# Kernel tuning notes

Hardware: AMD Instinct MI355X
Metric: run time of the kernel (lower is better)

## Reference

```python
import jax, jax.numpy as jnp
import numpy as np

B, S, DIM, N_CONCEPTS, N_LAYERS = 4, 2048, 1024, 2048, 2


def _phase_linear(x, W, b):
    # x: [b,s,d_in,2]; same real linear applied to real and imag components
    return jnp.einsum('bsdp,od->bsop', x, W) + b[:, None]


def _phase_layernorm(x, gamma, beta, eps=1e-5):
    # per-component LayerNorm over the feature dim with shared affine params
    mu = x.mean(axis=-2, keepdims=True)
    var = x.var(axis=-2, keepdims=True)
    return (x - mu) / jnp.sqrt(var + eps) * gamma[:, None] + beta[:, None]


def setup_inputs() -> dict:
    key = jax.random.key(0)
    ks = jax.random.split(key, 8)
    x = jax.random.normal(ks[0], (B, S, DIM, 2), dtype=jnp.float32)
    concept_memory = jax.random.normal(ks[1], (N_CONCEPTS, DIM, 2), dtype=jnp.float32) * 0.02
    scale = 1.0 / np.sqrt(DIM)
    W_layers = jax.random.normal(ks[2], (N_LAYERS, DIM, DIM), dtype=jnp.float32) * scale
    b_layers = jnp.zeros((N_LAYERS, DIM), dtype=jnp.float32)
    gamma = jnp.ones((N_LAYERS, DIM), dtype=jnp.float32)
    beta = jnp.zeros((N_LAYERS, DIM), dtype=jnp.float32)
    W_out = jax.random.normal(ks[3], (DIM, DIM), dtype=jnp.float32) * scale
    b_out = jnp.zeros((DIM,), dtype=jnp.float32)
    g_out = jnp.ones((DIM,), dtype=jnp.float32)
    beta_out = jnp.zeros((DIM,), dtype=jnp.float32)
    return {"x": x, "concept_memory": concept_memory, "W_layers": W_layers,
            "b_layers": b_layers, "gamma": gamma, "beta": beta,
            "W_out": W_out, "b_out": b_out, "g_out": g_out, "beta_out": beta_out}


def reference(x, concept_memory, W_layers, b_layers, gamma, beta, W_out, b_out, g_out, beta_out):
    xr, xi = x[..., 0], x[..., 1]                       # [b,s,d]
    cr, ci = concept_memory[..., 0], concept_memory[..., 1]  # [n,d]
    # phase-coherence concept attention
    dot_real = jnp.einsum('bsd,nd->bsn', xr, cr) + jnp.einsum('bsd,nd->bsn', xi, ci)
    x_mag = jnp.sqrt((xr ** 2 + xi ** 2).sum(axis=-1, keepdims=True) + 1e-8)   # [b,s,1]
    c_mag = jnp.sqrt((cr ** 2 + ci ** 2).sum(axis=-1) + 1e-8)                  # [n]
    coherence = dot_real / (x_mag * c_mag[None, None, :] + 1e-8)
    concept_attn = jax.nn.softmax(coherence * 2.0, axis=-1)
    concept_retrieved = jnp.einsum('bsn,ndp->bsdp', concept_attn, concept_memory)
    h = x + concept_retrieved * 0.1
    # gated FFN blocks (eval mode: dropout off)
    for l in range(N_LAYERS):
        residual = h
        h = _phase_layernorm(h, gamma[l], beta[l])
        h = _phase_linear(h, W_layers[l], b_layers[l])
        h = jax.nn.gelu(h[..., 0:1], approximate=False) * h
        h = residual + h * 0.1
    out = _phase_layernorm(h, g_out, beta_out)
    out = _phase_linear(out, W_out, b_out)
    return out
```

## Files before the change

kernel.cpp:

```cpp
#include <hip/hip_runtime.h>
#include <hip/hip_bf16.h>

#define ROWS 8192
#define K2   2048
#define NCPT 2048
#define DIMD 1024

using short8 = __attribute__((ext_vector_type(8))) short;
using f32x4  = __attribute__((ext_vector_type(4))) float;

__device__ __forceinline__ unsigned short f2b(float f) {
  __hip_bfloat16 h = __float2bfloat16(f);
  return *reinterpret_cast<unsigned short*>(&h);
}
__device__ __forceinline__ float b2f(unsigned short u) {
  unsigned int x = ((unsigned int)u) << 16;
  return __uint_as_float(x);
}

__device__ __forceinline__ void store_bf16x8(unsigned short* dst, const float4& a, const float4& b) {
  union { unsigned short u[8]; uint4 q; } p;
  p.u[0]=f2b(a.x); p.u[1]=f2b(a.y); p.u[2]=f2b(a.z); p.u[3]=f2b(a.w);
  p.u[4]=f2b(b.x); p.u[5]=f2b(b.y); p.u[6]=f2b(b.z); p.u[7]=f2b(b.w);
  *reinterpret_cast<uint4*>(dst) = p.q;
}
__device__ __forceinline__ void store_bf16x4(unsigned short* dst, float a, float b, float c, float d) {
  union { unsigned short u[4]; uint2 q; } p;
  p.u[0]=f2b(a); p.u[1]=f2b(b); p.u[2]=f2b(c); p.u[3]=f2b(d);
  *reinterpret_cast<uint2*>(dst) = p.q;
}

__device__ __forceinline__ void async_lds16(const void* g, void* l) {
  __builtin_amdgcn_global_load_lds((__attribute__((address_space(1))) void*)g,
                                   (__attribute__((address_space(3))) void*)l, 16, 0, 0);
}

__global__ void cast_row_mag(const float* __restrict__ src, unsigned short* __restrict__ dst,
                             float* __restrict__ mag, int ncol) {
  __shared__ float sred[4];
  int row = blockIdx.x, t = threadIdx.x;
  const float* s = src + (size_t)row * ncol;
  unsigned short* d = dst + (size_t)row * ncol;
  float ss = 0.f;
  for (int i = t * 8; i < ncol; i += 2048) {
    float4 a = *(const float4*)(s + i);
    float4 b = *(const float4*)(s + i + 4);
    ss += a.x*a.x + a.y*a.y + a.z*a.z + a.w*a.w;
    ss += b.x*b.x + b.y*b.y + b.z*b.z + b.w*b.w;
    store_bf16x8(d + i, a, b);
  }
  int lane = t & 63, w = t >> 6;
  for (int o = 32; o; o >>= 1) ss += __shfl_down(ss, o);
  if (lane == 0) sred[w] = ss;
  __syncthreads();
  if (t == 0) mag[row] = sqrtf(sred[0] + sred[1] + sred[2] + sred[3] + 1e-8f);
}

__global__ void cast_w(const float* __restrict__ wl, const float* __restrict__ wo,
                       unsigned short* __restrict__ dst) {
  int b = blockIdx.x;
  const float* src;
  unsigned short* d;
  if (b < 1024) { src = wl + (size_t)b * 2048; d = dst + (size_t)b * 2048; }
  else {
    src = wo + (size_t)(b - 1024) * 2048;
    d = dst + (size_t)2 * 1024 * 1024 + (size_t)(b - 1024) * 2048;
  }
  int i = threadIdx.x * 8;
  float4 a = *(const float4*)(src + i);
  float4 c = *(const float4*)(src + i + 4);
  store_bf16x8(d + i, a, c);
}

__global__ void transpose_f2b(const float* __restrict__ src, unsigned short* __restrict__ dst, int n) {
  __shared__ float tile[32][33];
  int bx = blockIdx.x * 32;
  int by = blockIdx.y * 32;
  int tx = threadIdx.x & 31, ty = threadIdx.x >> 5;
  #pragma unroll
  for (int i = ty; i < 32; i += 8)
    tile[i][tx] = src[(size_t)(by + i) * n + bx + tx];
  __syncthreads();
  #pragma unroll
  for (int i = ty; i < 32; i += 8)
    dst[(size_t)(bx + i) * n + by + tx] = f2b(tile[tx][i]);
}

__global__ void softmax_attn(const unsigned short* __restrict__ logit, unsigned short* __restrict__ attn) {
  __shared__ float sred[4];
  int row = blockIdx.x, t = threadIdx.x;
  int lane = t & 63, w = t >> 6;
  const unsigned short* lr = logit + (size_t)row * NCPT + t * 8;
  short8 lv = *reinterpret_cast<const short8*>(lr);
  float l[8];
  #pragma unroll
  for (int i = 0; i < 8; ++i) l[i] = b2f((unsigned short)lv[i]);
  float m = l[0];
  #pragma unroll
  for (int i = 1; i < 8; ++i) m = fmaxf(m, l[i]);
  for (int o = 32; o; o >>= 1) m = fmaxf(m, __shfl_down(m, o));
  if (lane == 0) sred[w] = m;
  __syncthreads();
  m = fmaxf(fmaxf(sred[0], sred[1]), fmaxf(sred[2], sred[3]));
  __syncthreads();
  float e[8], s = 0.f;
  #pragma unroll
  for (int i = 0; i < 8; ++i) { e[i] = expf(l[i] - m); s += e[i]; }
  for (int o = 32; o; o >>= 1) s += __shfl_down(s, o);
  if (lane == 0) sred[w] = s;
  __syncthreads();
  s = sred[0] + sred[1] + sred[2] + sred[3];
  float inv = 1.f / s;
  float4 A = make_float4(e[0]*inv, e[1]*inv, e[2]*inv, e[3]*inv);
  float4 B = make_float4(e[4]*inv, e[5]*inv, e[6]*inv, e[7]*inv);
  store_bf16x8(attn + (size_t)row * NCPT + t * 8, A, B);
}

__global__ void phase_ln(const unsigned short* __restrict__ h, const float* __restrict__ gamma,
                         const float* __restrict__ beta, unsigned short* __restrict__ out) {
  __shared__ float4 s4[4];
  int bs = blockIdx.x, t = threadIdx.x;
  const unsigned short* hr = h + (size_t)bs * 2048 + t * 8;
  short8 hv = *reinterpret_cast<const short8*>(hr);
  float r0 = b2f((unsigned short)hv[0]), i0 = b2f((unsigned short)hv[1]);
  float r1 = b2f((unsigned short)hv[2]), i1 = b2f((unsigned short)hv[3]);
  float r2 = b2f((unsigned short)hv[4]), i2 = b2f((unsigned short)hv[5]);
  float r3 = b2f((unsigned short)hv[6]), i3 = b2f((unsigned short)hv[7]);
  float4 s;
  s.x = r0 + r1 + r2 + r3;
  s.y = r0*r0 + r1*r1 + r2*r2 + r3*r3;
  s.z = i0 + i1 + i2 + i3;
  s.w = i0*i0 + i1*i1 + i2*i2 + i3*i3;
  int lane = t & 63, w = t >> 6;
  for (int o = 32; o; o >>= 1) {
    s.x += __shfl_down(s.x, o); s.y += __shfl_down(s.y, o);
    s.z += __shfl_down(s.z, o); s.w += __shfl_down(s.w, o);
  }
  if (lane == 0) s4[w] = s;
  __syncthreads();
  float4 T = s4[0];
  #pragma unroll
  for (int i = 1; i < 4; ++i) { T.x += s4[i].x; T.y += s4[i].y; T.z += s4[i].z; T.w += s4[i].w; }
  const float invd = 1.f / 1024.f;
  float mu_r = T.x * invd, var_r = T.y * invd - mu_r * mu_r;
  float mu_i = T.z * invd, var_i = T.w * invd - mu_i * mu_i;
  float is_r = 1.f / sqrtf(var_r + 1e-5f);
  float is_i = 1.f / sqrtf(var_i + 1e-5f);
  float4 g = *(const float4*)(gamma + t * 4);
  float4 b = *(const float4*)(beta + t * 4);
  unsigned short* o0 = out + (size_t)(2 * bs) * 1024 + t * 4;
  unsigned short* o1 = out + (size_t)(2 * bs + 1) * 1024 + t * 4;
  store_bf16x4(o0, (r0-mu_r)*is_r*g.x + b.x, (r1-mu_r)*is_r*g.y + b.y,
                   (r2-mu_r)*is_r*g.z + b.z, (r3-mu_r)*is_r*g.w + b.w);
  store_bf16x4(o1, (i0-mu_i)*is_i*g.x + b.x, (i1-mu_i)*is_i*g.y + b.y,
                   (i2-mu_i)*is_i*g.z + b.z, (i3-mu_i)*is_i*g.w + b.w);
}

template <int EPI>
__global__ __launch_bounds__(512, 2) void gemm256(
    const unsigned short* __restrict__ A, const unsigned short* __restrict__ B,
    int M, int N, int K, void* __restrict__ Cv, const float* __restrict__ aux,
    const float* __restrict__ aux2, const unsigned short* __restrict__ auxb) {
  __shared__ char lds[131072];
  const int t = threadIdx.x;
  const int l = t & 63;
  const int wid = t >> 6;
  const int wm = wid >> 2, wn = wid & 3;

  const int nwg = gridDim.x * gridDim.y;
  int bid = blockIdx.y * gridDim.x + blockIdx.x;
  const int chunk = nwg >> 3;
  bid = (bid & 7) * chunk + (bid >> 3);
  const int row0 = (bid / gridDim.x) * 256;
  const int col0 = (bid % gridDim.x) * 256;

  const int NT = K >> 6;
  const int l15 = l & 15, l7 = l & 7, lk = l >> 4;

  f32x4 acc[8][4] = {};
  short8 afA[4][2];
  short8 bfA[2][2];
  short8 bfB[2][2];

  auto stage = [&](const unsigned short* gmat, int tileRow, int kcol, char* region) {
    const int rsub = t >> 3;
    const int csw = ((t & 7) ^ (rsub & 7)) << 3;
    const unsigned short* g0 = gmat + (size_t)(tileRow + rsub) * K + kcol + csw;
    async_lds16(g0, region + (t & ~63) * 16);
    async_lds16(g0 + (size_t)64 * K, region + 8192 + (t & ~63) * 16);
  };

  auto rdA = [&](const char* base, int m, int kh) -> short8 {
    const int r = wm * 64 + m * 16 + l15;
    const int sp = ((((kh << 2) | lk) ^ l7) << 4);
    return *reinterpret_cast<const short8*>(base + r * 128 + sp);
  };
  auto rdB = [&](const char* base, int n, int kh) -> short8 {
    const int r = wn * 32 + n * 16 + l15;
    const int sp = ((((kh << 2) | lk) ^ l7) << 4);
    return *reinterpret_cast<const short8*>(base + r * 128 + sp);
  };

  stage(A, row0,       0, lds + 0);
  stage(A, row0 + 128, 0, lds + 16384);
  stage(B, col0,       0, lds + 32768);
  stage(B, col0 + 128, 0, lds + 49152);
  if (NT > 1) {
    stage(A, row0,       64, lds + 65536 + 0);
    stage(A, row0 + 128, 64, lds + 65536 + 16384);
    stage(B, col0,       64, lds + 65536 + 32768);
    stage(B, col0 + 128, 64, lds + 65536 + 49152);
    asm volatile("s_waitcnt vmcnt(8)" ::: "memory");
  } else {
    asm volatile("s_waitcnt vmcnt(0)" ::: "memory");
  }
  __builtin_amdgcn_s_barrier();
  asm volatile("" ::: "memory");

  #pragma unroll
  for (int n = 0; n < 2; ++n)
    #pragma unroll
    for (int kh = 0; kh < 2; ++kh)
      bfA[n][kh] = rdB(lds + 32768, n, kh);

  for (int tk = 0; tk < NT; ++tk) {
    char* bufC = lds + (tk & 1) * 65536;
    char* bufN = lds + (((tk + 1) & 1) * 65536);
    const bool pf = (tk + 2 < NT);
    const int kpf = (tk + 2) * 64;

    #pragma unroll
    for (int m = 0; m < 4; ++m)
      #pragma unroll
      for (int kh = 0; kh < 2; ++kh)
        afA[m][kh] = rdA(bufC + 0, m, kh);
    __builtin_amdgcn_s_setprio(1);
    #pragma unroll
    for (int kh = 0; kh < 2; ++kh)
      #pragma unroll
      for (int m = 0; m < 4; ++m)
        #pragma unroll
        for (int n = 0; n < 2; ++n)
          acc[m][n] = __builtin_amdgcn_mfma_f32_16x16x32_bf16(afA[m][kh], bfA[n][kh], acc[m][n], 0, 0, 0);
    __builtin_amdgcn_s_setprio(0);
    #pragma unroll
    for (int n = 0; n < 2; ++n)
      #pragma unroll
      for (int kh = 0; kh < 2; ++kh)
        bfB[n][kh] = rdB(bufC + 49152, n, kh);
    asm volatile("" ::: "memory");
    __builtin_amdgcn_s_barrier();
    asm volatile("" ::: "memory");

    __builtin_amdgcn_s_setprio(1);
    #pragma unroll
    for (int kh = 0; kh < 2; ++kh)
      #pragma unroll
      for (int m = 0; m < 4; ++m)
        #pragma unroll
        for (int n = 0; n < 2; ++n)
          acc[m][n + 2] = __builtin_amdgcn_mfma_f32_16x16x32_bf16(afA[m][kh], bfB[n][kh], acc[m][n + 2], 0, 0, 0);
    __builtin_amdgcn_s_setprio(0);
    if (pf) {
      stage(A, row0, kpf, bufC + 0);
      stage(B, col0, kpf, bufC + 32768);
    }
    asm volatile("" ::: "memory");
    __builtin_amdgcn_s_barrier();
    asm volatile("" ::: "memory");

    #pragma unroll
    for (int m = 0; m < 4; ++m)
      #pragma unroll
      for (int kh = 0; kh < 2; ++kh)
        afA[m][kh] = rdA(bufC + 16384, m, kh);
    __builtin_amdgcn_s_setprio(1);
    #pragma unroll
    for (int kh = 0; kh < 2; ++kh)
      #pragma unroll
      for (int m = 0; m < 4; ++m)
        #pragma unroll
        for (int n = 0; n < 2; ++n)
          acc[m + 4][n] = __builtin_amdgcn_mfma_f32_16x16x32_bf16(afA[m][kh], bfA[n][kh], acc[m + 4][n], 0, 0, 0);
    __builtin_amdgcn_s_setprio(0);
    if (pf) stage(B, col0 + 128, kpf, bufC + 49152);
    asm volatile("" ::: "memory");
    __builtin_amdgcn_s_barrier();
    asm volatile("" ::: "memory");

    __builtin_amdgcn_s_setprio(1);
    #pragma unroll
    for (int kh = 0; kh < 2; ++kh)
      #pragma unroll
      for (int m = 0; m < 4; ++m)
        #pragma unroll
        for (int n = 0; n < 2; ++n)
          acc[m + 4][n + 2] = __builtin_amdgcn_mfma_f32_16x16x32_bf16(afA[m][kh], bfB[n][kh], acc[m + 4][n + 2], 0, 0, 0);
    __builtin_amdgcn_s_setprio(0);
    if (pf) stage(A, row0 + 128, kpf, bufC + 16384);
    if (tk + 1 < NT) {
      #pragma unroll
      for (int n = 0; n < 2; ++n)
        #pragma unroll
        for (int kh = 0; kh < 2; ++kh)
          bfA[n][kh] = rdB(bufN + 32768, n, kh);
    }
    if (pf) {
      asm volatile("s_waitcnt vmcnt(4)" ::: "memory");
    } else {
      asm volatile("s_waitcnt vmcnt(0)" ::: "memory");
    }
    __builtin_amdgcn_s_barrier();
    asm volatile("" ::: "memory");
  }
  asm volatile("s_waitcnt vmcnt(0)" ::: "memory");

  const int cr = lk * 4;
  #pragma unroll
  for (int m = 0; m < 8; ++m) {
    const int gr = row0 + ((m >> 2) << 7) + wm * 64 + ((m & 3) << 4) + cr;
    #pragma unroll
    for (int n = 0; n < 4; ++n) {
      const int gc = col0 + ((n >> 1) << 7) + wn * 32 + ((n & 1) << 4) + l15;
      if constexpr (EPI == 0) {
        unsigned short* C = (unsigned short*)Cv;
        const float cm_ = aux2[gc];
        #pragma unroll
        for (int j = 0; j < 4; ++j) {
          const int r = gr + j;
          float v = 2.f * acc[m][n][j] / (aux[r] * cm_ + 1e-8f);
          C[(size_t)r * N + gc] = f2b(v);
        }
      } else if constexpr (EPI == 1) {
        unsigned short* C = (unsigned short*)Cv;
        #pragma unroll
        for (int j = 0; j < 4; ++j) {
          const int r = gr + j;
          C[(size_t)r * N + gc] = f2b(b2f(auxb[(size_t)r * N + gc]) + 0.1f * acc[m][n][j]);
        }
      } else if constexpr (EPI == 2) {
        unsigned short* C = (unsigned short*)Cv;
        const float bb = aux[gc];
        #pragma unroll
        for (int jj = 0; jj < 2; ++jj) {
          const int r = gr + jj * 2;
          float re = acc[m][n][jj * 2] + bb;
          float im = acc[m][n][jj * 2 + 1] + bb;
          float g = 0.5f * re * (1.f + erff(re * 0.70710678118654752440f));
          size_t idx = (size_t)(r >> 1) * 2048 + (size_t)gc * 2;
          unsigned int hv = *(unsigned int*)(C + idx);
          float hx = b2f((unsigned short)(hv & 0xffff));
          float hy = b2f((unsigned short)(hv >> 16));
          hx += 0.1f * g * re;
          hy += 0.1f * g * im;
          unsigned int packed = (unsigned int)f2b(hx) | ((unsigned int)f2b(hy) << 16);
          *(unsigned int*)(C + idx) = packed;
        }
      } else {
        float* C = (float*)Cv;
        const float bb = aux[gc];
        const size_t idx0 = (size_t)(gr >> 1) * 2048 + (size_t)gc * 2;
        float2 v01 = make_float2(acc[m][n][0] + bb, acc[m][n][1] + bb);
        float2 v23 = make_float2(acc[m][n][2] + bb, acc[m][n][3] + bb);
        *(float2*)(C + idx0) = v01;
        *(float2*)(C + idx0 + 2048) = v23;
      }
    }
  }
}

extern "C" void kernel_launch(void* const* d_in, const int* in_sizes, int n_in,
                              void* d_out, int out_size, void* d_ws, size_t ws_size,
                              hipStream_t stream) {
  const float* x     = (const float*)d_in[0];
  const float* cm    = (const float*)d_in[1];
  const float* Wl    = (const float*)d_in[2];
  const float* bl    = (const float*)d_in[3];
  const float* gamma = (const float*)d_in[4];
  const float* beta  = (const float*)d_in[5];
  const float* Wo    = (const float*)d_in[6];
  const float* bo    = (const float*)d_in[7];
  const float* go    = (const float*)d_in[8];
  const float* bto   = (const float*)d_in[9];
  float* out = (float*)d_out;

  char* p = (char*)d_ws;
  unsigned short* x_bf = (unsigned short*)p; p += (size_t)ROWS * K2 * 2;
  unsigned short* c_bf = (unsigned short*)p; p += (size_t)NCPT * K2 * 2;
  unsigned short* c_T  = (unsigned short*)p; p += (size_t)K2 * NCPT * 2;
  unsigned short* w_bf = (unsigned short*)p; p += (size_t)3 * 1024 * 1024 * 2;
  float* x_mag = (float*)p; p += (size_t)ROWS * 4;
  float* c_mag = (float*)p; p += (size_t)NCPT * 4;
  unsigned short* dot_bf = (unsigned short*)p; p += (size_t)ROWS * NCPT * 2;
  unsigned short* attn   = (unsigned short*)p; p += (size_t)ROWS * NCPT * 2;
  unsigned short* h      = (unsigned short*)p; p += (size_t)ROWS * K2 * 2;
  unsigned short* ln_bf = attn;

  cast_row_mag<<<ROWS, 256, 0, stream>>>(x, x_bf, x_mag, K2);
  cast_row_mag<<<NCPT, 256, 0, stream>>>(cm, c_bf, c_mag, K2);
  transpose_f2b<<<dim3(64, 64), 256, 0, stream>>>(cm, c_T, 2048);
  cast_w<<<1536, 256, 0, stream>>>(Wl, Wo, w_bf);

  gemm256<0><<<dim3(NCPT / 256, ROWS / 256), 512, 0, stream>>>(
      x_bf, c_bf, ROWS, NCPT, K2, dot_bf, x_mag, c_mag, nullptr);
  softmax_attn<<<ROWS, 256, 0, stream>>>(dot_bf, attn);
  gemm256<1><<<dim3(K2 / 256, ROWS / 256), 512, 0, stream>>>(
      attn, c_T, ROWS, K2, NCPT, h, nullptr, nullptr, x_bf);

  for (int l = 0; l < 2; ++l) {
    phase_ln<<<ROWS, 256, 0, stream>>>(h, gamma + l * 1024, beta + l * 1024, ln_bf);
    gemm256<2><<<dim3(DIMD / 256, 2 * ROWS / 256), 512, 0, stream>>>(
        ln_bf, w_bf + (size_t)l * 1024 * 1024, 2 * ROWS, DIMD, DIMD, h, bl + l * 1024, nullptr, nullptr);
  }

  phase_ln<<<ROWS, 256, 0, stream>>>(h, go, bto, ln_bf);
  gemm256<3><<<dim3(DIMD / 256, 2 * ROWS / 256), 512, 0, stream>>>(
      ln_bf, w_bf + 2 * 1024 * 1024, 2 * ROWS, DIMD, DIMD, out, bo, nullptr, nullptr);
}
```

Measured before the change: 362.5 us.

## Restructure GEMM main loop into eight-phase ping-pong with explicit LDS waits

Reworks the 256x256 bf16 MFMA GEMM main loop so each of the four quadrant MFMA blocks is preceded by its own LDS reads and global prefetch stage, separated by barriers with explicit lgkmcnt waits and sched_barrier fences. The B-fragment preload across iterations is removed; B fragments are now read from the current buffer at the start of each iteration. The aim is a tighter ping-pong schedule where memory issue and MFMA bursts alternate between wave groups. It adds more barriers per iteration and changes the vmcnt wait count, which could add synchronization stalls.

```diff
diff --git a/kernel.cpp b/kernel.cpp
--- a/kernel.cpp
+++ b/kernel.cpp
@@ -178,9 +178,9 @@
   const int l15 = l & 15, l7 = l & 7, lk = l >> 4;
 
   f32x4 acc[8][4] = {};
-  short8 afA[4][2];
-  short8 bfA[2][2];
-  short8 bfB[2][2];
+  short8 a_[4][2];
+  short8 b0_[2][2];
+  short8 b1_[2][2];
 
   auto stage = [&](const unsigned short* gmat, int tileRow, int kcol, char* region) {
     const int rsub = t >> 3;
@@ -217,15 +217,8 @@
   __builtin_amdgcn_s_barrier();
   asm volatile("" ::: "memory");
 
-  #pragma unroll
-  for (int n = 0; n < 2; ++n)
-    #pragma unroll
-    for (int kh = 0; kh < 2; ++kh)
-      bfA[n][kh] = rdB(lds + 32768, n, kh);
-
   for (int tk = 0; tk < NT; ++tk) {
     char* bufC = lds + (tk & 1) * 65536;
-    char* bufN = lds + (((tk + 1) & 1) * 65536);
     const bool pf = (tk + 2 < NT);
     const int kpf = (tk + 2) * 64;
 
@@ -233,7 +226,16 @@
     for (int m = 0; m < 4; ++m)
       #pragma unroll
       for (int kh = 0; kh < 2; ++kh)
-        afA[m][kh] = rdA(bufC + 0, m, kh);
+        a_[m][kh] = rdA(bufC + 0, m, kh);
+    #pragma unroll
+    for (int n = 0; n < 2; ++n)
+      #pragma unroll
+      for (int kh = 0; kh < 2; ++kh)
+        b0_[n][kh] = rdB(bufC + 32768, n, kh);
+    asm volatile("s_waitcnt lgkmcnt(8)" ::: "memory");
+    __builtin_amdgcn_s_barrier();
+    asm volatile("s_waitcnt lgkmcnt(0)" ::: "memory");
+    __builtin_amdgcn_sched_barrier(0);
     __builtin_amdgcn_s_setprio(1);
     #pragma unroll
     for (int kh = 0; kh < 2; ++kh)
@@ -241,30 +243,33 @@
       for (int m = 0; m < 4; ++m)
         #pragma unroll
         for (int n = 0; n < 2; ++n)
-          acc[m][n] = __builtin_amdgcn_mfma_f32_16x16x32_bf16(afA[m][kh], bfA[n][kh], acc[m][n], 0, 0, 0);
+          acc[m][n] = __builtin_amdgcn_mfma_f32_16x16x32_bf16(a_[m][kh], b0_[n][kh], acc[m][n], 0, 0, 0);
     __builtin_amdgcn_s_setprio(0);
+    asm volatile("" ::: "memory");
+    __builtin_amdgcn_s_barrier();
+    asm volatile("" ::: "memory");
+
     #pragma unroll
     for (int n = 0; n < 2; ++n)
       #pragma unroll
       for (int kh = 0; kh < 2; ++kh)
-        bfB[n][kh] = rdB(bufC + 49152, n, kh);
-    asm volatile("" ::: "memory");
-    __builtin_amdgcn_s_barrier();
-    asm volatile("" ::: "memory");
-
-    __builtin_amdgcn_s_setprio(1);
-    #pragma unroll
-    for (int kh = 0; kh < 2; ++kh)
-      #pragma unroll
-      for (int m = 0; m < 4; ++m)
-        #pragma unroll
-        for (int n = 0; n < 2; ++n)
-          acc[m][n + 2] = __builtin_amdgcn_mfma_f32_16x16x32_bf16(afA[m][kh], bfB[n][kh], acc[m][n + 2], 0, 0, 0);
-    __builtin_amdgcn_s_setprio(0);
+        b1_[n][kh] = rdB(bufC + 49152, n, kh);
     if (pf) {
       stage(A, row0, kpf, bufC + 0);
       stage(B, col0, kpf, bufC + 32768);
     }
+    __builtin_amdgcn_s_barrier();
+    asm volatile("s_waitcnt lgkmcnt(0)" ::: "memory");
+    __builtin_amdgcn_sched_barrier(0);
+    __builtin_amdgcn_s_setprio(1);
+    #pragma unroll
+    for (int kh = 0; kh < 2; ++kh)
+      #pragma unroll
+      for (int m = 0; m < 4; ++m)
+        #pragma unroll
+        for (int n = 0; n < 2; ++n)
+          acc[m][n + 2] = __builtin_amdgcn_mfma_f32_16x16x32_bf16(a_[m][kh], b1_[n][kh], acc[m][n + 2], 0, 0, 0);
+    __builtin_amdgcn_s_setprio(0);
     asm volatile("" ::: "memory");
     __builtin_amdgcn_s_barrier();
     asm volatile("" ::: "memory");
@@ -273,7 +278,11 @@
     for (int m = 0; m < 4; ++m)
       #pragma unroll
       for (int kh = 0; kh < 2; ++kh)
-        afA[m][kh] = rdA(bufC + 16384, m, kh);
+        a_[m][kh] = rdA(bufC + 16384, m, kh);
+    if (pf) stage(B, col0 + 128, kpf, bufC + 49152);
+    __builtin_amdgcn_s_barrier();
+    asm volatile("s_waitcnt lgkmcnt(0)" ::: "memory");
+    __builtin_amdgcn_sched_barrier(0);
     __builtin_amdgcn_s_setprio(1);
     #pragma unroll
     for (int kh = 0; kh < 2; ++kh)
@@ -281,35 +290,30 @@
       for (int m = 0; m < 4; ++m)
         #pragma unroll
         for (int n = 0; n < 2; ++n)
-          acc[m + 4][n] = __builtin_amdgcn_mfma_f32_16x16x32_bf16(afA[m][kh], bfA[n][kh], acc[m + 4][n], 0, 0, 0);
+          acc[m + 4][n] = __builtin_amdgcn_mfma_f32_16x16x32_bf16(a_[m][kh], b0_[n][kh], acc[m + 4][n], 0, 0, 0);
     __builtin_amdgcn_s_setprio(0);
-    if (pf) stage(B, col0 + 128, kpf, bufC + 49152);
-    asm volatile("" ::: "memory");
-    __builtin_amdgcn_s_barrier();
-    asm volatile("" ::: "memory");
-
-    __builtin_amdgcn_s_setprio(1);
-    #pragma unroll
-    for (int kh = 0; kh < 2; ++kh)
-      #pragma unroll
-      for (int m = 0; m < 4; ++m)
-        #pragma unroll
-        for (int n = 0; n < 2; ++n)
-          acc[m + 4][n + 2] = __builtin_amdgcn_mfma_f32_16x16x32_bf16(afA[m][kh], bfB[n][kh], acc[m + 4][n + 2], 0, 0, 0);
-    __builtin_amdgcn_s_setprio(0);
-    if (pf) stage(A, row0 + 128, kpf, bufC + 16384);
-    if (tk + 1 < NT) {
-      #pragma unroll
-      for (int n = 0; n < 2; ++n)
-        #pragma unroll
-        for (int kh = 0; kh < 2; ++kh)
-          bfA[n][kh] = rdB(bufN + 32768, n, kh);
-    }
+    asm volatile("" ::: "memory");
+    __builtin_amdgcn_s_barrier();
+    asm volatile("" ::: "memory");
+
     if (pf) {
-      asm volatile("s_waitcnt vmcnt(4)" ::: "memory");
+      stage(A, row0 + 128, kpf, bufC + 16384);
+      asm volatile("s_waitcnt vmcnt(6)" ::: "memory");
     } else {
       asm volatile("s_waitcnt vmcnt(0)" ::: "memory");
     }
+    __builtin_amdgcn_s_barrier();
+    asm volatile("" ::: "memory");
+    __builtin_amdgcn_s_setprio(1);
+    #pragma unroll
+    for (int kh = 0; kh < 2; ++kh)
+      #pragma unroll
+      for (int m = 0; m < 4; ++m)
+        #pragma unroll
+        for (int n = 0; n < 2; ++n)
+          acc[m + 4][n + 2] = __builtin_amdgcn_mfma_f32_16x16x32_bf16(a_[m][kh], b1_[n][kh], acc[m + 4][n + 2], 0, 0, 0);
+    __builtin_amdgcn_s_setprio(0);
+    asm volatile("" ::: "memory");
     __builtin_amdgcn_s_barrier();
     asm volatile("" ::: "memory");
   }
```

Measured after the change: 390.4 us. +7.7%, slower.

## Run concept attention GEMMs in FP8 with scaled MFMA

Applied to the files above, without the earlier changes.

Converts x, the concept memory, its transpose and the softmax attention weights to FP8 e4m3, with power-of-two prescales (16 for concepts, 256 for attention) undone in the epilogues. Adds a new gemm256f8 kernel that uses the 16x16x128 f8f6f4 scaled MFMA with 128-wide K tiles, replacing the two bf16 GEMMs of the attention stage. This halves operand bytes and raises matrix throughput, at the cost of reduced precision in the coherence logits and in the retrieved concepts.

```diff
diff --git a/kernel.cpp b/kernel.cpp
--- a/kernel.cpp
+++ b/kernel.cpp
@@ -1,5 +1,6 @@
 #include <hip/hip_runtime.h>
 #include <hip/hip_bf16.h>
+#include <hip/hip_fp8.h>
 
 #define ROWS 8192
 #define K2   2048
@@ -8,6 +9,7 @@
 
 using short8 = __attribute__((ext_vector_type(8))) short;
 using f32x4  = __attribute__((ext_vector_type(4))) float;
+using int8v  = __attribute__((ext_vector_type(8))) int;
 
 __device__ __forceinline__ unsigned short f2b(float f) {
   __hip_bfloat16 h = __float2bfloat16(f);
@@ -16,6 +18,10 @@
 __device__ __forceinline__ float b2f(unsigned short u) {
   unsigned int x = ((unsigned int)u) << 16;
   return __uint_as_float(x);
+}
+__device__ __forceinline__ unsigned char f2f8(float f) {
+  __hip_fp8_e4m3 h(f);
+  return (unsigned char)h.__x;
 }
 
 __device__ __forceinline__ void store_bf16x8(unsigned short* dst, const float4& a, const float4& b) {
@@ -29,25 +35,32 @@
   p.u[0]=f2b(a); p.u[1]=f2b(b); p.u[2]=f2b(c); p.u[3]=f2b(d);
   *reinterpret_cast<uint2*>(dst) = p.q;
 }
+__device__ __forceinline__ void store_fp8x8(unsigned char* dst, const float4& a, const float4& b, float s) {
+  union { unsigned char c[8]; uint2 q; } p;
+  p.c[0]=f2f8(a.x*s); p.c[1]=f2f8(a.y*s); p.c[2]=f2f8(a.z*s); p.c[3]=f2f8(a.w*s);
+  p.c[4]=f2f8(b.x*s); p.c[5]=f2f8(b.y*s); p.c[6]=f2f8(b.z*s); p.c[7]=f2f8(b.w*s);
+  *reinterpret_cast<uint2*>(dst) = p.q;
+}
 
 __device__ __forceinline__ void async_lds16(const void* g, void* l) {
   __builtin_amdgcn_global_load_lds((__attribute__((address_space(1))) void*)g,
                                    (__attribute__((address_space(3))) void*)l, 16, 0, 0);
 }
 
-__global__ void cast_row_mag(const float* __restrict__ src, unsigned short* __restrict__ dst,
+__global__ void cast_row_mag(const float* __restrict__ src, unsigned short* __restrict__ dst_bf,
+                             unsigned char* __restrict__ dst_f8, float fscale,
                              float* __restrict__ mag, int ncol) {
   __shared__ float sred[4];
   int row = blockIdx.x, t = threadIdx.x;
   const float* s = src + (size_t)row * ncol;
-  unsigned short* d = dst + (size_t)row * ncol;
   float ss = 0.f;
   for (int i = t * 8; i < ncol; i += 2048) {
     float4 a = *(const float4*)(s + i);
     float4 b = *(const float4*)(s + i + 4);
     ss += a.x*a.x + a.y*a.y + a.z*a.z + a.w*a.w;
     ss += b.x*b.x + b.y*b.y + b.z*b.z + b.w*b.w;
-    store_bf16x8(d + i, a, b);
+    if (dst_bf) store_bf16x8(dst_bf + (size_t)row * ncol + i, a, b);
+    store_fp8x8(dst_f8 + (size_t)row * ncol + i, a, b, fscale);
   }
   int lane = t & 63, w = t >> 6;
   for (int o = 32; o; o >>= 1) ss += __shfl_down(ss, o);
@@ -72,7 +85,7 @@
   store_bf16x8(d + i, a, c);
 }
 
-__global__ void transpose_f2b(const float* __restrict__ src, unsigned short* __restrict__ dst, int n) {
+__global__ void transpose_f8(const float* __restrict__ src, unsigned char* __restrict__ dst, int n) {
   __shared__ float tile[32][33];
   int bx = blockIdx.x * 32;
   int by = blockIdx.y * 32;
@@ -83,10 +96,10 @@
   __syncthreads();
   #pragma unroll
   for (int i = ty; i < 32; i += 8)
-    dst[(size_t)(bx + i) * n + by + tx] = f2b(tile[tx][i]);
-}
-
-__global__ void softmax_attn(const unsigned short* __restrict__ logit, unsigned short* __restrict__ attn) {
+    dst[(size_t)(bx + i) * n + by + tx] = f2f8(16.f * tile[tx][i]);
+}
+
+__global__ void softmax_attn(const unsigned short* __restrict__ logit, unsigned char* __restrict__ attn) {
   __shared__ float sred[4];
   int row = blockIdx.x, t = threadIdx.x;
   int lane = t & 63, w = t >> 6;
@@ -110,10 +123,10 @@
   if (lane == 0) sred[w] = s;
   __syncthreads();
   s = sred[0] + sred[1] + sred[2] + sred[3];
-  float inv = 1.f / s;
+  float inv = 256.f / s;
   float4 A = make_float4(e[0]*inv, e[1]*inv, e[2]*inv, e[3]*inv);
   float4 B = make_float4(e[4]*inv, e[5]*inv, e[6]*inv, e[7]*inv);
-  store_bf16x8(attn + (size_t)row * NCPT + t * 8, A, B);
+  store_fp8x8(attn + (size_t)row * NCPT + t * 8, A, B, 1.f);
 }
 
 __global__ void phase_ln(const unsigned short* __restrict__ h, const float* __restrict__ gamma,
@@ -322,23 +335,7 @@
     #pragma unroll
     for (int n = 0; n < 4; ++n) {
       const int gc = col0 + ((n >> 1) << 7) + wn * 32 + ((n & 1) << 4) + l15;
-      if constexpr (EPI == 0) {
-        unsigned short* C = (unsigned short*)Cv;
-        const float cm_ = aux2[gc];
-        #pragma unroll
-        for (int j = 0; j < 4; ++j) {
-          const int r = gr + j;
-          float v = 2.f * acc[m][n][j] / (aux[r] * cm_ + 1e-8f);
-          C[(size_t)r * N + gc] = f2b(v);
-        }
-      } else if constexpr (EPI == 1) {
-        unsigned short* C = (unsigned short*)Cv;
-        #pragma unroll
-        for (int j = 0; j < 4; ++j) {
-          const int r = gr + j;
-          C[(size_t)r * N + gc] = f2b(b2f(auxb[(size_t)r * N + gc]) + 0.1f * acc[m][n][j]);
-        }
-      } else if constexpr (EPI == 2) {
+      if constexpr (EPI == 2) {
         unsigned short* C = (unsigned short*)Cv;
         const float bb = aux[gc];
         #pragma unroll
@@ -369,6 +366,178 @@
   }
 }
 
+template <int EPI8>
+__global__ __launch_bounds__(512, 2) void gemm256f8(
+    const unsigned char* __restrict__ A, const unsigned char* __restrict__ B,
+    int M, int N, int K, void* __restrict__ Cv, const float* __restrict__ aux,
+    const float* __restrict__ aux2, const unsigned short* __restrict__ auxb) {
+  __shared__ char lds[131072];
+  const int t = threadIdx.x;
+  const int l = t & 63;
+  const int wid = t >> 6;
+  const int wm = wid >> 2, wn = wid & 3;
+
+  const int nwg = gridDim.x * gridDim.y;
+  int bid = blockIdx.y * gridDim.x + blockIdx.x;
+  const int chunk = nwg >> 3;
+  bid = (bid & 7) * chunk + (bid >> 3);
+  const int row0 = (bid / gridDim.x) * 256;
+  const int col0 = (bid % gridDim.x) * 256;
+
+  const int NT = K >> 7;
+  const int l15 = l & 15, l7 = l & 7, lk = l >> 4;
+
+  f32x4 acc[8][4] = {};
+  int8v a8[4];
+  int8v b0_[2];
+  int8v b1_[2];
+
+  auto stage = [&](const unsigned char* gmat, int tileRow, int kcol, char* region) {
+    const int rsub = t >> 3;
+    const int csw = ((t & 7) ^ (rsub & 7)) << 4;
+    const unsigned char* g0 = gmat + (size_t)(tileRow + rsub) * K + kcol + csw;
+    async_lds16(g0, region + (t & ~63) * 16);
+    async_lds16(g0 + (size_t)64 * K, region + 8192 + (t & ~63) * 16);
+  };
+
+  auto rdA8 = [&](const char* base, int m) -> int8v {
+    union { int8v v; uint4 q[2]; } u;
+    const int r = wm * 64 + m * 16 + l15;
+    u.q[0] = *(const uint4*)(base + r * 128 + ((((lk << 1) | 0) ^ l7) << 4));
+    u.q[1] = *(const uint4*)(base + r * 128 + ((((lk << 1) | 1) ^ l7) << 4));
+    return u.v;
+  };
+  auto rdB8 = [&](const char* base, int n) -> int8v {
+    union { int8v v; uint4 q[2]; } u;
+    const int r = wn * 32 + n * 16 + l15;
+    u.q[0] = *(const uint4*)(base + r * 128 + ((((lk << 1) | 0) ^ l7) << 4));
+    u.q[1] = *(const uint4*)(base + r * 128 + ((((lk << 1) | 1) ^ l7) << 4));
+    return u.v;
+  };
+
+  #define MFMA8(AF, BF, CC) \
+    __builtin_amdgcn_mfma_scale_f32_16x16x128_f8f6f4(AF, BF, CC, 0, 0, 0, 0x7F7F7F7F, 0, 0x7F7F7F7F)
+
+  stage(A, row0,       0, lds + 0);
+  stage(A, row0 + 128, 0, lds + 16384);
+  stage(B, col0,       0, lds + 32768);
+  stage(B, col0 + 128, 0, lds + 49152);
+  if (NT > 1) {
+    stage(A, row0,       128, lds + 65536 + 0);
+    stage(A, row0 + 128, 128, lds + 65536 + 16384);
+    stage(B, col0,       128, lds + 65536 + 32768);
+    stage(B, col0 + 128, 128, lds + 65536 + 49152);
+    asm volatile("s_waitcnt vmcnt(8)" ::: "memory");
+  } else {
+    asm volatile("s_waitcnt vmcnt(0)" ::: "memory");
+  }
+  __builtin_amdgcn_s_barrier();
+  asm volatile("" ::: "memory");
+
+  #pragma unroll
+  for (int n = 0; n < 2; ++n) b0_[n] = rdB8(lds + 32768, n);
+
+  for (int tk = 0; tk < NT; ++tk) {
+    char* bufC = lds + (tk & 1) * 65536;
+    char* bufN = lds + (((tk + 1) & 1) * 65536);
+    const bool pf = (tk + 2 < NT);
+    const int kpf = (tk + 2) * 128;
+
+    #pragma unroll
+    for (int m = 0; m < 4; ++m) a8[m] = rdA8(bufC + 0, m);
+    __builtin_amdgcn_s_setprio(1);
+    #pragma unroll
+    for (int m = 0; m < 4; ++m)
+      #pragma unroll
+      for (int n = 0; n < 2; ++n)
+        acc[m][n] = MFMA8(a8[m], b0_[n], acc[m][n]);
+    __builtin_amdgcn_s_setprio(0);
+    #pragma unroll
+    for (int n = 0; n < 2; ++n) b1_[n] = rdB8(bufC + 49152, n);
+    asm volatile("" ::: "memory");
+    __builtin_amdgcn_s_barrier();
+    asm volatile("" ::: "memory");
+
+    __builtin_amdgcn_s_setprio(1);
+    #pragma unroll
+    for (int m = 0; m < 4; ++m)
+      #pragma unroll
+      for (int n = 0; n < 2; ++n)
+        acc[m][n + 2] = MFMA8(a8[m], b1_[n], acc[m][n + 2]);
+    __builtin_amdgcn_s_setprio(0);
+    if (pf) {
+      stage(A, row0, kpf, bufC + 0);
+      stage(B, col0, kpf, bufC + 32768);
+    }
+    asm volatile("" ::: "memory");
+    __builtin_amdgcn_s_barrier();
+    asm volatile("" ::: "memory");
+
+    #pragma unroll
+    for (int m = 0; m < 4; ++m) a8[m] = rdA8(bufC + 16384, m);
+    __builtin_amdgcn_s_setprio(1);
+    #pragma unroll
+    for (int m = 0; m < 4; ++m)
+      #pragma unroll
+      for (int n = 0; n < 2; ++n)
+        acc[m + 4][n] = MFMA8(a8[m], b0_[n], acc[m + 4][n]);
+    __builtin_amdgcn_s_setprio(0);
+    if (pf) stage(B, col0 + 128, kpf, bufC + 49152);
+    asm volatile("" ::: "memory");
+    __builtin_amdgcn_s_barrier();
+    asm volatile("" ::: "memory");
+
+    __builtin_amdgcn_s_setprio(1);
+    #pragma unroll
+    for (int m = 0; m < 4; ++m)
+      #pragma unroll
+      for (int n = 0; n < 2; ++n)
+        acc[m + 4][n + 2] = MFMA8(a8[m], b1_[n], acc[m + 4][n + 2]);
+    __builtin_amdgcn_s_setprio(0);
+    if (pf) stage(A, row0 + 128, kpf, bufC + 16384);
+    if (tk + 1 < NT) {
+      #pragma unroll
+      for (int n = 0; n < 2; ++n) b0_[n] = rdB8(bufN + 32768, n);
+    }
+    if (pf) {
+      asm volatile("s_waitcnt vmcnt(4)" ::: "memory");
+    } else {
+      asm volatile("s_waitcnt vmcnt(0)" ::: "memory");
+    }
+    __builtin_amdgcn_s_barrier();
+    asm volatile("" ::: "memory");
+  }
+  asm volatile("s_waitcnt vmcnt(0)" ::: "memory");
+  #undef MFMA8
+
+  const int cr = lk * 4;
+  #pragma unroll
+  for (int m = 0; m < 8; ++m) {
+    const int gr = row0 + ((m >> 2) << 7) + wm * 64 + ((m & 3) << 4) + cr;
+    #pragma unroll
+    for (int n = 0; n < 4; ++n) {
+      const int gc = col0 + ((n >> 1) << 7) + wn * 32 + ((n & 1) << 4) + l15;
+      if constexpr (EPI8 == 0) {
+        unsigned short* C = (unsigned short*)Cv;
+        const float cm_ = aux2[gc];
+        #pragma unroll
+        for (int j = 0; j < 4; ++j) {
+          const int r = gr + j;
+          float v = 0.125f * acc[m][n][j] / (aux[r] * cm_ + 1e-8f);
+          C[(size_t)r * N + gc] = f2b(v);
+        }
+      } else {
+        unsigned short* C = (unsigned short*)Cv;
+        #pragma unroll
+        for (int j = 0; j < 4; ++j) {
+          const int r = gr + j;
+          C[(size_t)r * N + gc] = f2b(b2f(auxb[(size_t)r * N + gc]) + 2.44140625e-5f * acc[m][n][j]);
+        }
+      }
+    }
+  }
+}
+
 extern "C" void kernel_launch(void* const* d_in, const int* in_sizes, int n_in,
                               void* d_out, int out_size, void* d_ws, size_t ws_size,
                               hipStream_t stream) {
@@ -385,27 +554,28 @@
   float* out = (float*)d_out;
 
   char* p = (char*)d_ws;
-  unsigned short* x_bf = (unsigned short*)p; p += (size_t)ROWS * K2 * 2;
-  unsigned short* c_bf = (unsigned short*)p; p += (size_t)NCPT * K2 * 2;
-  unsigned short* c_T  = (unsigned short*)p; p += (size_t)K2 * NCPT * 2;
-  unsigned short* w_bf = (unsigned short*)p; p += (size_t)3 * 1024 * 1024 * 2;
+  unsigned short* x_bf  = (unsigned short*)p; p += (size_t)ROWS * K2 * 2;
+  unsigned char*  x_f8  = (unsigned char*)p;  p += (size_t)ROWS * K2;
+  unsigned char*  c_f8  = (unsigned char*)p;  p += (size_t)NCPT * K2;
+  unsigned char*  cT_f8 = (unsigned char*)p;  p += (size_t)K2 * NCPT;
+  unsigned short* w_bf  = (unsigned short*)p; p += (size_t)3 * 1024 * 1024 * 2;
   float* x_mag = (float*)p; p += (size_t)ROWS * 4;
   float* c_mag = (float*)p; p += (size_t)NCPT * 4;
   unsigned short* dot_bf = (unsigned short*)p; p += (size_t)ROWS * NCPT * 2;
-  unsigned short* attn   = (unsigned short*)p; p += (size_t)ROWS * NCPT * 2;
+  unsigned char*  attn_f8 = (unsigned char*)p; p += (size_t)ROWS * NCPT;
   unsigned short* h      = (unsigned short*)p; p += (size_t)ROWS * K2 * 2;
-  unsigned short* ln_bf = attn;
-
-  cast_row_mag<<<ROWS, 256, 0, stream>>>(x, x_bf, x_mag, K2);
-  cast_row_mag<<<NCPT, 256, 0, stream>>>(cm, c_bf, c_mag, K2);
-  transpose_f2b<<<dim3(64, 64), 256, 0, stream>>>(cm, c_T, 2048);
+  unsigned short* ln_bf = dot_bf;
+
+  cast_row_mag<<<ROWS, 256, 0, stream>>>(x, x_bf, x_f8, 1.f, x_mag, K2);
+  cast_row_mag<<<NCPT, 256, 0, stream>>>(cm, nullptr, c_f8, 16.f, c_mag, K2);
+  transpose_f8<<<dim3(64, 64), 256, 0, stream>>>(cm, cT_f8, 2048);
   cast_w<<<1536, 256, 0, stream>>>(Wl, Wo, w_bf);
 
-  gemm256<0><<<dim3(NCPT / 256, ROWS / 256), 512, 0, stream>>>(
-      x_bf, c_bf, ROWS, NCPT, K2, dot_bf, x_mag, c_mag, nullptr);
-  softmax_attn<<<ROWS, 256, 0, stream>>>(dot_bf, attn);
-  gemm256<1><<<dim3(K2 / 256, ROWS / 256), 512, 0, stream>>>(
-      attn, c_T, ROWS, K2, NCPT, h, nullptr, nullptr, x_bf);
+  gemm256f8<0><<<dim3(NCPT / 256, ROWS / 256), 512, 0, stream>>>(
+      x_f8, c_f8, ROWS, NCPT, K2, dot_bf, x_mag, c_mag, nullptr);
+  softmax_attn<<<ROWS, 256, 0, stream>>>(dot_bf, attn_f8);
+  gemm256f8<1><<<dim3(K2 / 256, ROWS / 256), 512, 0, stream>>>(
+      attn_f8, cT_f8, ROWS, K2, NCPT, h, nullptr, nullptr, x_bf);
 
   for (int l = 0; l < 2; ++l) {
     phase_ln<<<ROWS, 256, 0, stream>>>(h, gamma + l * 1024, beta + l * 1024, ln_bf);
```

New measurement: 364.4 us. About the same (+0.5%).
